# Kernel tuning notes

Hardware: AMD Instinct MI355X
Metric: run time of the kernel (lower is better)

## Reference

```python
import jax, jax.numpy as jnp
import numpy as np

POS_THR = 0.5      # ROI_POSITIVE_THR
NEG_THR = 0.1      # ROI_NEGATIVE_THR
N_SAMPLES = 256    # ROI_SAMPLES
FG_RATIO = 0.25    # ROI_SAMPLE_RATIO
L1W = 1.0          # RPN.L1WEIGHT_INTERSECTION
NUM_FG = int(N_SAMPLES * FG_RATIO)


def _make_boxes(kxy, kwh, shape):
    # valid [x1,y1,x2,y2] boxes in an ~800px image
    xy = jax.random.uniform(kxy, shape[:-1] + (2,)) * 800.0
    wh = jax.random.uniform(kwh, shape[:-1] + (2,)) * 200.0 + 1.0
    return jnp.concatenate([xy, xy + wh], axis=-1)


def setup_inputs() -> dict:
    key = jax.random.key(0)
    k1, k2, k3, k4 = jax.random.split(key, 4)
    proposals = _make_boxes(k1, k2, (16, 16384, 4))  # [B, N, 4]
    gt_boxes = _make_boxes(k3, k4, (16, 128, 4))     # [B, G, 4]
    return {"proposals": proposals, "gt_boxes": gt_boxes}


def _centrehw(b):
    # [x1,y1,x2,y2] -> [cx,cy,w,h]
    x1, y1, x2, y2 = b[..., 0], b[..., 1], b[..., 2], b[..., 3]
    return jnp.stack([(x1 + x2) * 0.5, (y1 + y2) * 0.5, x2 - x1, y2 - y1], axis=-1)


def _targets(gt_c, roi_c):
    dx = (gt_c[..., 0] - roi_c[..., 0]) / roi_c[..., 2]
    dy = (gt_c[..., 1] - roi_c[..., 1]) / roi_c[..., 3]
    dw = jnp.log(gt_c[..., 2] / roi_c[..., 2])
    dh = jnp.log(gt_c[..., 3] / roi_c[..., 3])
    return jnp.stack([dx, dy, dw, dh], axis=-1)


def _iou(prop, gt):
    # prop [B,N,4], gt [B,G,4] -> IoU [B,N,G]
    p = prop[:, :, None, :]
    g = gt[:, None, :, :]
    ix1 = jnp.maximum(p[..., 0], g[..., 0])
    iy1 = jnp.maximum(p[..., 1], g[..., 1])
    ix2 = jnp.minimum(p[..., 2], g[..., 2])
    iy2 = jnp.minimum(p[..., 3], g[..., 3])
    inter = jnp.clip(ix2 - ix1, 0.0) * jnp.clip(iy2 - iy1, 0.0)
    ap = (p[..., 2] - p[..., 0]) * (p[..., 3] - p[..., 1])
    ag = (g[..., 2] - g[..., 0]) * (g[..., 3] - g[..., 1])
    return inter / jnp.maximum(ap + ag - inter, 1e-8)


def _forward(proposals, gt_boxes):
    B, N, _ = proposals.shape
    iou = _iou(proposals, gt_boxes)                       # [B,N,G]
    max_iou = iou.max(axis=-1)                            # [B,N]
    argmax_gt = iou.argmax(axis=-1).astype(jnp.int32)     # [B,N]
    # classify: 1=fg, 0=bg, -1=ignore
    labels = jnp.where(max_iou >= POS_THR, 1,
                       jnp.where(max_iou < NEG_THR, 0, -1)).astype(jnp.int32)
    # randsample: keep <= NUM_FG positives (random), fill rest with negatives.
    r = jax.random.uniform(jax.random.key(1), (B, N))
    pos = labels == 1
    r_pos = jnp.where(pos, r, -1.0)
    order = jnp.argsort(-r_pos, axis=1)
    ranks = jnp.argsort(order, axis=1)                    # rank among positives by r
    pos_sel = pos & (ranks < NUM_FG)
    prio = jnp.where(pos_sel, 3.0 + r,
                     jnp.where(labels == 0, 2.0 + r,
                               jnp.where(pos, 1.0 + r, r)))
    _, idx = jax.lax.top_k(prio, N_SAMPLES)               # [B,S] sampled proposal ids
    batch_labels = jnp.maximum(jnp.take_along_axis(labels, idx, axis=1), 0)  # [B,S]
    roi_batch = jnp.take_along_axis(proposals, idx[..., None], axis=1)       # [B,S,4]
    sel_gt = jnp.take_along_axis(argmax_gt, idx, axis=1)                     # [B,S]
    gt_batch = jnp.take_along_axis(gt_boxes, sel_gt[..., None], axis=1)      # [B,S,4]
    bbox_targets = _targets(_centrehw(gt_batch), _centrehw(roi_batch))       # [B,S,4]
    in_w = jnp.where((batch_labels == 1)[..., None], L1W, 0.0)
    in_w = jnp.broadcast_to(in_w, bbox_targets.shape)
    out_w = (in_w > 0).astype(jnp.float32)
    return roi_batch, batch_labels, bbox_targets, in_w, out_w


def reference(proposals, gt_boxes):
    return _forward(proposals, gt_boxes)
```

## Files before the change

### kernel.cpp

```cpp
#include <hip/hip_runtime.h>
#include <stdint.h>

#define BATCH 16
#define NPROP 16384
#define NGT   128
#define NSAMP 256
#define NFG   64
#define GCAP  512
#define PCAP  8192
#define HCAP  2048
#define NBLK  128
#define BPB   128
#define NEGT  0x780002u

typedef unsigned long long ull;

__device__ __forceinline__ void thr_block(uint32_t c0, uint32_t c1,
                                          uint32_t* o0, uint32_t* o1) {
    const uint32_t k0 = 0u, k1 = 1u, ks2 = 0x1BD11BDBu;
    uint32_t x0 = c0 + k0, x1 = c1 + k1;
#define RND(d) { x0 += x1; x1 = (x1 << d) | (x1 >> (32 - d)); x1 ^= x0; }
    RND(13) RND(15) RND(26) RND(6)   x0 += k1;  x1 += ks2 + 1u;
    RND(17) RND(29) RND(16) RND(24)  x0 += ks2; x1 += k0 + 2u;
    RND(13) RND(15) RND(26) RND(6)   x0 += k0;  x1 += k1 + 3u;
    RND(17) RND(29) RND(16) RND(24)  x0 += k1;  x1 += ks2 + 4u;
    RND(13) RND(15) RND(26) RND(6)   x0 += ks2; x1 += k0 + 5u;
#undef RND
    *o0 = x0; *o1 = x1;
}

__device__ __forceinline__ uint32_t thr_part_xor(uint32_t f) {
    uint32_t a, b; thr_block(0u, f, &a, &b);
    return a ^ b;
}

__global__ void __launch_bounds__(256) k_compute(
    const float* __restrict__ props, const float* __restrict__ gts,
    ull* __restrict__ lists, uint32_t* __restrict__ cntblk)
{
#pragma clang fp contract(off)
    const int b = blockIdx.y;
    const int blk = blockIdx.x;
    const int tid = threadIdx.x;
    const int half = tid & 1;
    const int n = blk * BPB + (tid >> 1);
    __shared__ float2 sA[130];
    __shared__ float2 sB[130];
    __shared__ float  sag[130];
    __shared__ uint32_t wc[4][4], we_s[4][4];
    if (tid < NGT) {
        float4 g = ((const float4*)gts)[(size_t)b * NGT + tid];
        int idx = (tid < 64) ? tid : tid + 1;
        sA[idx] = make_float2(g.x, g.y);
        sB[idx] = make_float2(g.z, g.w);
        sag[idx] = (g.z - g.x) * (g.w - g.y);
    }
    __syncthreads();
    const float4 pb = ((const float4*)props)[(size_t)b * NPROP + n];
    const float ap = (pb.z - pb.x) * (pb.w - pb.y);
    float best = -1.0f; int bg = 0;
    const int base  = half ? 65 : 0;
    const int gbias = half ? 64 : 0;
    #pragma unroll 4
    for (int i = 0; i < 64; ++i) {
        const float2 a = sA[base + i];
        const float2 c = sB[base + i];
        float w  = fmaxf(fminf(pb.z, c.x) - fmaxf(pb.x, a.x), 0.0f);
        float hh = fmaxf(fminf(pb.w, c.y) - fmaxf(pb.y, a.y), 0.0f);
        float inter = w * hh;
        float un = fmaxf(ap + sag[base + i] - inter, 1e-8f);
        float iou = inter / un;
        if (iou > best) { best = iou; bg = gbias + i; }
    }
    float ob = __shfl_xor(best, 1);
    int  obg = __shfl_xor(bg, 1);
    if (half == 0 && ob > best) { best = ob; bg = obg; }

    uint32_t lab = (best >= 0.5f) ? 2u : ((best < 0.1f) ? 1u : 0u);
    const uint32_t f = (uint32_t)b * NPROP + (uint32_t)n;
    uint32_t mant = thr_part_xor(f) >> 9;
    ull entry = ((ull)(lab == 2u) << 44) | ((ull)mant << 21)
              | ((ull)(16383u - (uint32_t)n) << 7) | (ull)(uint32_t)bg;

    const bool isEven = (half == 0);
    bool cP = isEven && (lab == 2u);
    bool cH = isEven && (lab == 1u) && (mant >= NEGT);
    bool cL = isEven && (lab == 1u) && (mant <  NEGT);
    bool cI = isEven && (lab == 0u);
    ull mP = __ballot(cP), mH = __ballot(cH), mL = __ballot(cL), mI = __ballot(cI);
    const int w = tid >> 6;
    const uint32_t lane = (uint32_t)tid & 63u;
    if (lane == 0) {
        wc[0][w] = (uint32_t)__popcll(mP);
        wc[1][w] = (uint32_t)__popcll(mH);
        wc[2][w] = (uint32_t)__popcll(mL);
        wc[3][w] = (uint32_t)__popcll(mI);
    }
    __syncthreads();
    if (tid < 4) {
        uint32_t e = 0;
        #pragma unroll
        for (int i = 0; i < 4; i++) { we_s[tid][i] = e; e += wc[tid][i]; }
        cntblk[((size_t)b * NBLK + blk) * 4 + tid] = e;
    }
    __syncthreads();
    ull lt = lane ? (~0ull >> (64u - lane)) : 0ull;
    ull* slab = lists + (size_t)b * 4 * NPROP;
    const uint32_t segB = (uint32_t)blk * BPB;
    if (cP) slab[0 * NPROP + segB + we_s[0][w] + (uint32_t)__popcll(mP & lt)] = entry;
    if (cH) slab[1 * NPROP + segB + we_s[1][w] + (uint32_t)__popcll(mH & lt)] = entry;
    if (cL) slab[2 * NPROP + segB + we_s[2][w] + (uint32_t)__popcll(mL & lt)] = entry;
    if (cI) slab[3 * NPROP + segB + we_s[3][w] + (uint32_t)__popcll(mI & lt)] = entry;
}

__global__ void __launch_bounds__(1024) k_select(
    const float* __restrict__ props, const float* __restrict__ gts,
    const ull* __restrict__ lists, const uint32_t* __restrict__ cntblk,
    float* __restrict__ out)
{
#pragma clang fp contract(off)
    const int b = blockIdx.x;
    const int tid = threadIdx.x;
    const int wid = tid >> 6;
    const uint32_t lane = (uint32_t)tid & 63u;
    __shared__ ull      dpos[PCAP];
    __shared__ ull      dnh[HCAP];
    __shared__ uint32_t hist[2048];
    __shared__ ull      gat[GCAP];
    __shared__ ull      selk[NSAMP];
    __shared__ uint32_t sela[NSAMP];
    __shared__ uint32_t bc[NBLK * 4];
    __shared__ uint32_t tot[4];
    __shared__ uint32_t sh_dig, sh_k, sh_cnt_in, gcnt, selc, stP, stH;
    __shared__ ull sh_thr;

    const ull* Spos = lists + ((size_t)b * 4 + 0) * NPROP;
    const ull* SnH  = lists + ((size_t)b * 4 + 1) * NPROP;
    const ull* SnL  = lists + ((size_t)b * 4 + 2) * NPROP;
    const ull* Sign = lists + ((size_t)b * 4 + 3) * NPROP;
    if (tid < 4) tot[tid] = 0;
    if (tid == 0) { selc = 0; stP = 0; stH = 0; }
    __syncthreads();
    if (tid < NBLK * 4) {
        uint32_t v = cntblk[(size_t)b * NBLK * 4 + tid];
        bc[tid] = v;
        atomicAdd(&tot[tid & 3], v);
    }
    __syncthreads();
    const uint32_t npos = tot[0], nH = tot[1], nL = tot[2], nig = tot[3];
    const uint32_t nneg = nH + nL;
    const uint32_t npn  = npos + nneg;
    const bool dP = (npos <= PCAP), dH = (nH <= HCAP);

    {
        for (int s8 = 0; s8 < 8; ++s8) {
            uint32_t seg = (uint32_t)(wid * 8 + s8);
            if (dP) {
                uint32_t c = bc[seg * 4 + 0];
                for (uint32_t i0 = 0; i0 < c; i0 += 64) {
                    uint32_t take = (c - i0 < 64u) ? (c - i0) : 64u;
                    uint32_t s0 = 0;
                    if (lane == 0) s0 = atomicAdd(&stP, take);
                    s0 = (uint32_t)__shfl((int)s0, 0);
                    if (lane < take) dpos[s0 + lane] = Spos[seg * BPB + i0 + lane];
                }
            }
            if (dH) {
                uint32_t c = bc[seg * 4 + 1];
                for (uint32_t i0 = 0; i0 < c; i0 += 64) {
                    uint32_t take = (c - i0 < 64u) ? (c - i0) : 64u;
                    uint32_t s0 = 0;
                    if (lane == 0) s0 = atomicAdd(&stH, take);
                    s0 = (uint32_t)__shfl((int)s0, 0);
                    if (lane < take) dnh[s0 + lane] = SnH[seg * BPB + i0 + lane];
                }
            }
        }
    }
    __syncthreads();

    const uint32_t MSEG = NBLK * BPB;
    const uint32_t mPos = dP ? npos : MSEG;
    const uint32_t mH   = dH ? nH   : MSEG;
    auto posEnt = [&](uint32_t j, bool& e) -> ull {
        if (dP) { e = true; return dpos[j]; }
        e = (j & (BPB - 1u)) < bc[(j >> 7) * 4 + 0];
        return e ? Spos[j] : 0ull;
    };
    auto nhEnt = [&](uint32_t j, bool& e) -> ull {
        if (dH) { e = true; return dnh[j]; }
        e = (j & (BPB - 1u)) < bc[(j >> 7) * 4 + 1];
        return e ? SnH[j] : 0ull;
    };
    auto nlEnt = [&](uint32_t j, bool& e) -> ull {
        e = (j & (BPB - 1u)) < bc[(j >> 7) * 4 + 2];
        return e ? SnL[j] : 0ull;
    };
    auto igEnt = [&](uint32_t j, bool& e) -> ull {
        e = (j & (BPB - 1u)) < bc[(j >> 7) * 4 + 3];
        return e ? Sign[j] : 0ull;
    };

    auto keyA_of = [](ull e) -> ull {
        return (((e >> 21) & 0x7FFFFFull) << 14) | ((e >> 7) & 0x3FFFull);
    };

    auto locate = [&](uint32_t k) {
        if (tid < 64) {
            uint32_t cs = 0;
            if (lane < 32) {
                const uint32_t base = lane * 64u;
                #pragma unroll 8
                for (uint32_t i = 0; i < 64; i++)
                    cs += hist[base + ((i + lane) & 63u)];
            }
            uint32_t s = cs;
            #pragma unroll
            for (int off = 1; off < 32; off <<= 1) {
                uint32_t t = __shfl_down(s, off);
                if (lane + off < 32) s += t;
            }
            uint32_t sExcl = s - cs;
            bool cond = (lane < 32) && (sExcl < k) && (k <= s);
            ull ball = __ballot(cond);
            uint32_t cstar = (uint32_t)(__ffsll((unsigned long long)ball) - 1);
            uint32_t kc = (uint32_t)__shfl((int)(k - sExcl), (int)cstar);
            uint32_t val = hist[cstar * 64u + lane];
            uint32_t fi = val;
            #pragma unroll
            for (int off = 1; off < 64; off <<= 1) {
                uint32_t t = __shfl_down(fi, off);
                if (lane + off < 64) fi += t;
            }
            uint32_t fExcl = fi - val;
            bool cond2 = (fExcl < kc) && (kc <= fi);
            ull ball2 = __ballot(cond2);
            uint32_t bstar = (uint32_t)(__ffsll((unsigned long long)ball2) - 1);
            if (lane == bstar) {
                sh_dig = cstar * 64u + lane;
                sh_k = kc - fExcl;
                sh_cnt_in = val;
            }
        }
    };

    auto radix = [&](auto&& kf, uint32_t m, uint32_t k, int shift) -> ull {
        if (m <= GCAP) {
            if (tid == 0) gcnt = 0;
            __syncthreads();
            for (uint32_t j = tid; j < m; j += 1024) {
                bool e; ull key = kf(j, e);
                if (e) { uint32_t s = atomicAdd(&gcnt, 1u); gat[s] = key; }
            }
            __syncthreads();
            uint32_t gc = gcnt;
            if (tid < (int)gc) {
                ull x = gat[tid];
                uint32_t r = 0;
                for (uint32_t j = 0; j < gc; j++) r += (gat[j] > x);
                if (r == k - 1) sh_thr = x;
            }
            __syncthreads();
            return sh_thr;
        }
        ull prefix = 0, mask = 0;
        for (;;) {
            hist[tid] = 0; hist[tid + 1024] = 0;
            __syncthreads();
            for (uint32_t j = tid; j < m; j += 1024) {
                bool e; ull key = kf(j, e);
                if (e && ((key ^ prefix) & mask) == 0)
                    atomicAdd(&hist[(uint32_t)(key >> shift) & 2047u], 1u);
            }
            __syncthreads();
            locate(k);
            __syncthreads();
            uint32_t dig = sh_dig, kk = sh_k, cnt = sh_cnt_in;
            prefix |= ((ull)dig) << shift;
            mask   |= 2047ull << shift;
            if (cnt <= GCAP || shift == 0) {
                if (tid == 0) gcnt = 0;
                __syncthreads();
                for (uint32_t j = tid; j < m; j += 1024) {
                    bool e; ull key = kf(j, e);
                    if (e && ((key ^ prefix) & mask) == 0) {
                        uint32_t s = atomicAdd(&gcnt, 1u);
                        if (s < GCAP) gat[s] = key;
                    }
                }
                __syncthreads();
                uint32_t gc = (gcnt < GCAP) ? gcnt : GCAP;
                if (tid < (int)gc) {
                    ull x = gat[tid];
                    uint32_t r = 0;
                    for (uint32_t j = 0; j < gc; j++) r += (gat[j] > x);
                    if (r == kk - 1) sh_thr = x;
                }
                __syncthreads();
                return sh_thr;
            } else {
                k = kk;
                shift = (shift >= 11) ? shift - 11 : 0;
                __syncthreads();
            }
        }
    };

    ull thrA = 0;
    if (npos > NFG) {
        thrA = radix([&](uint32_t j, bool& e) -> ull {
            ull ent = posEnt(j, e); return keyA_of(ent); }, mPos, NFG, 26);
    }

    auto keyB_pos = [&](ull ent) -> ull {
        uint32_t mant = (uint32_t)((ent >> 21) & 0x7FFFFFull);
        uint32_t invn = (uint32_t)((ent >> 7) & 0x3FFFull);
        float r = __uint_as_float(0x3F800000u | mant) - 1.0f;
        uint32_t cls = (keyA_of(ent) >= thrA) ? 3u : 1u;
        float prio = (float)cls + r;
        return (((ull)__float_as_uint(prio)) << 14) | (ull)invn;
    };
    auto keyB_neg = [](ull ent) -> ull {
        uint32_t mant = (uint32_t)((ent >> 21) & 0x7FFFFFull);
        uint32_t invn = (uint32_t)((ent >> 7) & 0x3FFFull);
        float r = __uint_as_float(0x3F800000u | mant) - 1.0f;
        float prio = 2.0f + r;
        return (((ull)__float_as_uint(prio)) << 14) | (ull)invn;
    };
    auto keyB_ign = [](ull ent) -> ull {
        uint32_t mant = (uint32_t)((ent >> 21) & 0x7FFFFFull);
        uint32_t invn = (uint32_t)((ent >> 7) & 0x3FFFull);
        float r = __uint_as_float(0x3F800000u | mant) - 1.0f;
        float prio = 0.0f + r;
        return (((ull)__float_as_uint(prio)) << 14) | (ull)invn;
    };

    const uint32_t c3 = (npos < NFG) ? npos : NFG;
    const uint32_t c2 = nneg;
    uint32_t clsStar = (npn >= NSAMP) ? ((NSAMP <= c3 + c2) ? 2u : 1u) : 0u;
    bool scanL = true;
    const bool scanI = (clsStar == 0u);
    ull thrB = 0;
    if (clsStar == 2u) {
        uint32_t k2 = NSAMP - c3;
        if (nH >= k2) {
            scanL = false;
            thrB = radix([&](uint32_t j, bool& e) -> ull {
                ull ent = nhEnt(j, e); return keyB_neg(ent); }, mH, k2, 26);
        } else {
            thrB = radix([&](uint32_t j, bool& e) -> ull {
                if (j < mH) { ull ent = nhEnt(j, e); return keyB_neg(ent); }
                ull ent = nlEnt(j - mH, e); return keyB_neg(ent); },
                mH + MSEG, k2, 26);
        }
    } else if (clsStar == 1u) {
        thrB = radix([&](uint32_t j, bool& e) -> ull {
            ull ent = posEnt(j, e);
            ull kb = keyB_pos(ent);
            e = e && ((kb >> 14) < 0x40000000ull);
            return kb; }, mPos, NSAMP - c3 - c2, 26);
    } else {
        thrB = radix([&](uint32_t j, bool& e) -> ull {
            ull ent = igEnt(j, e); return keyB_ign(ent); }, MSEG, NSAMP - npn, 34);
    }
    __syncthreads();

    auto push = [&](ull key, ull ent, uint32_t fg) {
        uint32_t s = atomicAdd(&selc, 1u);
        if (s < NSAMP) { selk[s] = key; sela[s] = (fg << 7) | (uint32_t)(ent & 0x7Full); }
    };
    for (uint32_t j = tid; j < mPos; j += 1024) {
        bool e; ull ent = posEnt(j, e);
        if (!e) continue;
        ull key = keyB_pos(ent);
        if (clsStar == 0u || key >= thrB) push(key, ent, 1u);
    }
    for (uint32_t j = tid; j < mH; j += 1024) {
        bool e; ull ent = nhEnt(j, e);
        if (!e) continue;
        ull key = keyB_neg(ent);
        if (clsStar == 0u || key >= thrB) push(key, ent, 0u);
    }
    if (scanL) {
        for (uint32_t j = tid; j < MSEG; j += 1024) {
            bool e; ull ent = nlEnt(j, e);
            if (!e) continue;
            ull key = keyB_neg(ent);
            if (clsStar == 0u || key >= thrB) push(key, ent, 0u);
        }
    }
    if (scanI) {
        for (uint32_t j = tid; j < MSEG; j += 1024) {
            bool e; ull ent = igEnt(j, e);
            if (!e) continue;
            ull key = keyB_ign(ent);
            if (key >= thrB) push(key, ent, 0u);
        }
    }
    __syncthreads();

    if (tid < NSAMP) {
        ull x = selk[tid];
        uint32_t r = 0;
        for (int j = 0; j < NSAMP; j++) r += (selk[j] > x);
        uint32_t n = 16383u - (uint32_t)(x & 0x3FFFull);
        uint32_t aux = sela[tid];
        uint32_t bg = aux & 0x7Fu;
        const int isfg = (int)((aux >> 7) & 1u);
        const float4 pb = ((const float4*)props)[(size_t)b * NPROP + n];
        const float4 gb = ((const float4*)gts)[(size_t)b * NGT + bg];
        const size_t O_ROI = 0;
        const size_t O_LBL = (size_t)BATCH * NSAMP * 4;
        const size_t O_TGT = O_LBL + (size_t)BATCH * NSAMP;
        const size_t O_INW = O_TGT + (size_t)BATCH * NSAMP * 4;
        const size_t O_OUW = O_INW + (size_t)BATCH * NSAMP * 4;
        const size_t row = (size_t)b * NSAMP + r;
        out[O_ROI + row * 4 + 0] = pb.x;
        out[O_ROI + row * 4 + 1] = pb.y;
        out[O_ROI + row * 4 + 2] = pb.z;
        out[O_ROI + row * 4 + 3] = pb.w;
        out[O_LBL + row] = isfg ? 1.0f : 0.0f;
        float rw  = pb.z - pb.x, rh = pb.w - pb.y;
        float gw  = gb.z - gb.x, gh = gb.w - gb.y;
        out[O_TGT + row * 4 + 0] = ((gb.x + gb.z) * 0.5f - (pb.x + pb.z) * 0.5f) / rw;
        out[O_TGT + row * 4 + 1] = ((gb.y + gb.w) * 0.5f - (pb.y + pb.w) * 0.5f) / rh;
        out[O_TGT + row * 4 + 2] = logf(gw / rw);
        out[O_TGT + row * 4 + 3] = logf(gh / rh);
        float wv = isfg ? 1.0f : 0.0f;
        for (int c = 0; c < 4; c++) {
            out[O_INW + row * 4 + c] = wv;
            out[O_OUW + row * 4 + c] = wv;
        }
    }
}

extern "C" void kernel_launch(void* const* d_in, const int* in_sizes, int n_in,
                              void* d_out, int out_size, void* d_ws, size_t ws_size,
                              hipStream_t stream) {
    (void)in_sizes; (void)n_in; (void)out_size; (void)ws_size;
    const float* props = (const float*)d_in[0];
    const float* gts   = (const float*)d_in[1];
    ull* lists = (ull*)d_ws;
    uint32_t* cntblk = (uint32_t*)((char*)d_ws + (size_t)BATCH * 4 * NPROP * 8);
    float* out = (float*)d_out;

    dim3 gridA(NBLK, BATCH);
    k_compute<<<gridA, 256, 0, stream>>>(props, gts, lists, cntblk);
    k_select<<<BATCH, 1024, 0, stream>>>(props, gts, lists, cntblk, out);
}
```

Before: 103.9 us.

## Assign one proposal per thread instead of splitting GT boxes across lane pairs

The IoU kernel now gives each thread a whole proposal and loops over all 128 GT boxes, where before two lanes each scanned 64 boxes and merged with a shuffle. GT boxes are staged as raw float4 in shared memory and each box area is recomputed inside the loop. Blocks now cover 256 proposals, which halves the block count and changes the per-block segmentation used by the selection kernel. The select kernel sums totals with a serial loop over blocks instead of shared atomics. This removes the shuffle merge and the wasted odd lanes, at the cost of longer serial loops per thread and fewer blocks to spread across the device.

```diff
diff --git a/kernel.cpp b/kernel.cpp
--- a/kernel.cpp
+++ b/kernel.cpp
@@ -9,8 +9,9 @@
 #define GCAP  512
 #define PCAP  8192
 #define HCAP  2048
-#define NBLK  128
-#define BPB   128
+#define NBLK  64
+#define BPB   256
+#define LOGB  8
 #define NEGT  0x780002u
 
 typedef unsigned long long ull;
@@ -42,51 +43,36 @@
     const int b = blockIdx.y;
     const int blk = blockIdx.x;
     const int tid = threadIdx.x;
-    const int half = tid & 1;
-    const int n = blk * BPB + (tid >> 1);
-    __shared__ float2 sA[130];
-    __shared__ float2 sB[130];
-    __shared__ float  sag[130];
+    const int n = blk * BPB + tid;
+    __shared__ float4 g4[NGT];
     __shared__ uint32_t wc[4][4], we_s[4][4];
-    if (tid < NGT) {
-        float4 g = ((const float4*)gts)[(size_t)b * NGT + tid];
-        int idx = (tid < 64) ? tid : tid + 1;
-        sA[idx] = make_float2(g.x, g.y);
-        sB[idx] = make_float2(g.z, g.w);
-        sag[idx] = (g.z - g.x) * (g.w - g.y);
-    }
+    if (tid < NGT)
+        g4[tid] = ((const float4*)gts)[(size_t)b * NGT + tid];
     __syncthreads();
     const float4 pb = ((const float4*)props)[(size_t)b * NPROP + n];
     const float ap = (pb.z - pb.x) * (pb.w - pb.y);
     float best = -1.0f; int bg = 0;
-    const int base  = half ? 65 : 0;
-    const int gbias = half ? 64 : 0;
     #pragma unroll 4
-    for (int i = 0; i < 64; ++i) {
-        const float2 a = sA[base + i];
-        const float2 c = sB[base + i];
-        float w  = fmaxf(fminf(pb.z, c.x) - fmaxf(pb.x, a.x), 0.0f);
-        float hh = fmaxf(fminf(pb.w, c.y) - fmaxf(pb.y, a.y), 0.0f);
+    for (int i = 0; i < NGT; ++i) {
+        const float4 gb = g4[i];
+        float ag = (gb.z - gb.x) * (gb.w - gb.y);
+        float w  = fmaxf(fminf(pb.z, gb.z) - fmaxf(pb.x, gb.x), 0.0f);
+        float hh = fmaxf(fminf(pb.w, gb.w) - fmaxf(pb.y, gb.y), 0.0f);
         float inter = w * hh;
-        float un = fmaxf(ap + sag[base + i] - inter, 1e-8f);
+        float un = fmaxf(ap + ag - inter, 1e-8f);
         float iou = inter / un;
-        if (iou > best) { best = iou; bg = gbias + i; }
-    }
-    float ob = __shfl_xor(best, 1);
-    int  obg = __shfl_xor(bg, 1);
-    if (half == 0 && ob > best) { best = ob; bg = obg; }
-
+        if (iou > best) { best = iou; bg = i; }
+    }
     uint32_t lab = (best >= 0.5f) ? 2u : ((best < 0.1f) ? 1u : 0u);
     const uint32_t f = (uint32_t)b * NPROP + (uint32_t)n;
     uint32_t mant = thr_part_xor(f) >> 9;
     ull entry = ((ull)(lab == 2u) << 44) | ((ull)mant << 21)
               | ((ull)(16383u - (uint32_t)n) << 7) | (ull)(uint32_t)bg;
 
-    const bool isEven = (half == 0);
-    bool cP = isEven && (lab == 2u);
-    bool cH = isEven && (lab == 1u) && (mant >= NEGT);
-    bool cL = isEven && (lab == 1u) && (mant <  NEGT);
-    bool cI = isEven && (lab == 0u);
+    bool cP = (lab == 2u);
+    bool cH = (lab == 1u) && (mant >= NEGT);
+    bool cL = (lab == 1u) && (mant <  NEGT);
+    bool cI = (lab == 0u);
     ull mP = __ballot(cP), mH = __ballot(cH), mL = __ballot(cL), mI = __ballot(cI);
     const int w = tid >> 6;
     const uint32_t lane = (uint32_t)tid & 63u;
@@ -138,13 +124,13 @@
     const ull* SnH  = lists + ((size_t)b * 4 + 1) * NPROP;
     const ull* SnL  = lists + ((size_t)b * 4 + 2) * NPROP;
     const ull* Sign = lists + ((size_t)b * 4 + 3) * NPROP;
-    if (tid < 4) tot[tid] = 0;
     if (tid == 0) { selc = 0; stP = 0; stH = 0; }
-    __syncthreads();
-    if (tid < NBLK * 4) {
-        uint32_t v = cntblk[(size_t)b * NBLK * 4 + tid];
-        bc[tid] = v;
-        atomicAdd(&tot[tid & 3], v);
+    if (tid < NBLK * 4) bc[tid] = cntblk[(size_t)b * NBLK * 4 + tid];
+    __syncthreads();
+    if (tid < 4) {
+        uint32_t run = 0;
+        for (int blk = 0; blk < NBLK; ++blk) run += bc[blk * 4 + tid];
+        tot[tid] = run;
     }
     __syncthreads();
     const uint32_t npos = tot[0], nH = tot[1], nL = tot[2], nig = tot[3];
@@ -152,28 +138,26 @@
     const uint32_t npn  = npos + nneg;
     const bool dP = (npos <= PCAP), dH = (nH <= HCAP);
 
-    {
-        for (int s8 = 0; s8 < 8; ++s8) {
-            uint32_t seg = (uint32_t)(wid * 8 + s8);
-            if (dP) {
-                uint32_t c = bc[seg * 4 + 0];
-                for (uint32_t i0 = 0; i0 < c; i0 += 64) {
-                    uint32_t take = (c - i0 < 64u) ? (c - i0) : 64u;
-                    uint32_t s0 = 0;
-                    if (lane == 0) s0 = atomicAdd(&stP, take);
-                    s0 = (uint32_t)__shfl((int)s0, 0);
-                    if (lane < take) dpos[s0 + lane] = Spos[seg * BPB + i0 + lane];
-                }
-            }
-            if (dH) {
-                uint32_t c = bc[seg * 4 + 1];
-                for (uint32_t i0 = 0; i0 < c; i0 += 64) {
-                    uint32_t take = (c - i0 < 64u) ? (c - i0) : 64u;
-                    uint32_t s0 = 0;
-                    if (lane == 0) s0 = atomicAdd(&stH, take);
-                    s0 = (uint32_t)__shfl((int)s0, 0);
-                    if (lane < take) dnh[s0 + lane] = SnH[seg * BPB + i0 + lane];
-                }
+    for (int s4 = 0; s4 < 4; ++s4) {
+        uint32_t seg = (uint32_t)(wid * 4 + s4);
+        if (dP) {
+            uint32_t c = bc[seg * 4 + 0];
+            for (uint32_t i0 = 0; i0 < c; i0 += 64) {
+                uint32_t take = (c - i0 < 64u) ? (c - i0) : 64u;
+                uint32_t s0 = 0;
+                if (lane == 0) s0 = atomicAdd(&stP, take);
+                s0 = (uint32_t)__shfl((int)s0, 0);
+                if (lane < take) dpos[s0 + lane] = Spos[seg * BPB + i0 + lane];
+            }
+        }
+        if (dH) {
+            uint32_t c = bc[seg * 4 + 1];
+            for (uint32_t i0 = 0; i0 < c; i0 += 64) {
+                uint32_t take = (c - i0 < 64u) ? (c - i0) : 64u;
+                uint32_t s0 = 0;
+                if (lane == 0) s0 = atomicAdd(&stH, take);
+                s0 = (uint32_t)__shfl((int)s0, 0);
+                if (lane < take) dnh[s0 + lane] = SnH[seg * BPB + i0 + lane];
             }
         }
     }
@@ -184,20 +168,20 @@
     const uint32_t mH   = dH ? nH   : MSEG;
     auto posEnt = [&](uint32_t j, bool& e) -> ull {
         if (dP) { e = true; return dpos[j]; }
-        e = (j & (BPB - 1u)) < bc[(j >> 7) * 4 + 0];
+        e = (j & (BPB - 1u)) < bc[(j >> LOGB) * 4 + 0];
         return e ? Spos[j] : 0ull;
     };
     auto nhEnt = [&](uint32_t j, bool& e) -> ull {
         if (dH) { e = true; return dnh[j]; }
-        e = (j & (BPB - 1u)) < bc[(j >> 7) * 4 + 1];
+        e = (j & (BPB - 1u)) < bc[(j >> LOGB) * 4 + 1];
         return e ? SnH[j] : 0ull;
     };
     auto nlEnt = [&](uint32_t j, bool& e) -> ull {
-        e = (j & (BPB - 1u)) < bc[(j >> 7) * 4 + 2];
+        e = (j & (BPB - 1u)) < bc[(j >> LOGB) * 4 + 2];
         return e ? SnL[j] : 0ull;
     };
     auto igEnt = [&](uint32_t j, bool& e) -> ull {
-        e = (j & (BPB - 1u)) < bc[(j >> 7) * 4 + 3];
+        e = (j & (BPB - 1u)) < bc[(j >> LOGB) * 4 + 3];
         return e ? Sign[j] : 0ull;
     };
 
```

New measurement: 102.5 us. About the same (-1.4%).
